# Optimization experiments

Hardware: AMD Instinct MI355X
Metric: run time of the kernel (lower is better)

The kernel has to match this reference:

```python
import jax, jax.numpy as jnp
import numpy as np

BIG = jnp.float32(9e15)


def _normalize(sim, mask):
    # min/max are taken over positions where mask == 0 (faithful to the torch code)
    mn = jnp.min(jnp.where(mask == 0.0, sim, BIG), axis=-1, keepdims=True)
    mx = jnp.max(jnp.where(mask == 0.0, sim, -BIG), axis=-1, keepdims=True)
    return (sim - mn) / (mx - mn)


def setup_inputs() -> dict:
    key = jax.random.key(0)
    k1, k2 = jax.random.split(key)
    B, M = 4096, 8192
    return {
        "similarity_matrix": jax.random.normal(k1, (B, B), dtype=jnp.float32),
        "memory_bank_matrix": jax.random.normal(k2, (B, M), dtype=jnp.float32),
        "num_neighbors": 32,
        "temperature": jnp.ones((), dtype=jnp.float32),
    }


def reference(similarity_matrix, memory_bank_matrix, num_neighbors, temperature):
    sim = similarity_matrix
    B = sim.shape[0]
    eye = jnp.eye(B, dtype=sim.dtype)

    # --- neighbor masks via top-k over off-diagonal similarities ---
    sim_noself = jnp.where(eye == 0.0, sim, -BIG)
    _, topk_idx = jax.lax.top_k(sim_noself, num_neighbors)       # [B, k]
    rows = jnp.broadcast_to(jnp.arange(B)[:, None], topk_idx.shape)
    neighbor_mask = jnp.zeros((B, B), dtype=sim.dtype).at[rows, topk_idx].set(1.0)
    extended_mask = eye.at[rows, topk_idx].set(1.0)

    # --- centrality from memory bank ---
    centrality = jnp.mean(memory_bank_matrix, axis=-1)           # [B]
    cent_exp = jnp.broadcast_to(centrality[None, :], (B, B))

    norm_sim = _normalize(sim, extended_mask)
    norm_cent = _normalize(cent_exp, extended_mask)

    adjusted = jnp.where(neighbor_mask == 1.0, norm_sim - norm_cent, -BIG)

    # --- positive weights ---
    pw = jax.nn.softmax(adjusted * temperature, axis=-1)
    pw = jnp.where(neighbor_mask == 1.0, pw, 0.0)
    pw = jnp.where(eye == 1.0, 1.0, pw)  # fill_diagonal_(1.0)

    # --- masked log-softmax loss ---
    masked_sim = jnp.where(extended_mask == 1.0, sim, -BIG)
    logp = jax.nn.log_softmax(masked_sim, axis=-1) * pw
    per_row = -jnp.sum(logp, axis=-1) / jnp.sum(pw, axis=-1)
    return jnp.mean(per_row)
```

## Files before the change

kernel.cpp:

```cpp
#include <hip/hip_runtime.h>
#include <cmath>


#define CAP 256
#define MAXIT 40

__device__ inline float wave_max_f(float x) {
#pragma unroll
    for (int off = 32; off > 0; off >>= 1) x = fmaxf(x, __shfl_xor(x, off, 64));
    return x;
}
__device__ inline float wave_min_f(float x) {
#pragma unroll
    for (int off = 32; off > 0; off >>= 1) x = fminf(x, __shfl_xor(x, off, 64));
    return x;
}
__device__ inline float wave_sum_f(float x) {
#pragma unroll
    for (int off = 32; off > 0; off >>= 1) x += __shfl_xor(x, off, 64);
    return x;
}
__device__ inline unsigned int wave_min_u32(unsigned int x) {
#pragma unroll
    for (int off = 32; off > 0; off >>= 1) {
        unsigned int o = (unsigned int)__shfl_xor((int)x, off, 64);
        x = (o < x) ? o : x;
    }
    return x;
}

__device__ inline unsigned int f_to_key(float f) {
    unsigned int u = __float_as_uint(f);
    return u ^ ((u & 0x80000000u) ? 0xFFFFFFFFu : 0x80000000u);
}
__device__ inline float key_to_f(unsigned int key) {
    unsigned int u = key ^ ((key & 0x80000000u) ? 0x80000000u : 0xFFFFFFFFu);
    return __uint_as_float(u);
}

__global__ __launch_bounds__(256)
void cent_kernel(const float* __restrict__ mem, float* __restrict__ cent, int M) {
    __shared__ float s[4];
    const int row = blockIdx.x;
    const float4* p = (const float4*)(mem + (size_t)row * M);
    const int n4 = M >> 2;
    float acc = 0.0f;
    int i = threadIdx.x;
    for (; i + 1792 < n4; i += 2048) {
        float4 q0 = p[i], q1 = p[i + 256], q2 = p[i + 512], q3 = p[i + 768];
        float4 q4 = p[i + 1024], q5 = p[i + 1280], q6 = p[i + 1536], q7 = p[i + 1792];
        acc += ((q0.x + q0.y) + (q0.z + q0.w)) + ((q1.x + q1.y) + (q1.z + q1.w))
             + ((q2.x + q2.y) + (q2.z + q2.w)) + ((q3.x + q3.y) + (q3.z + q3.w))
             + ((q4.x + q4.y) + (q4.z + q4.w)) + ((q5.x + q5.y) + (q5.z + q5.w))
             + ((q6.x + q6.y) + (q6.z + q6.w)) + ((q7.x + q7.y) + (q7.z + q7.w));
    }
    for (; i < n4; i += 256) {
        float4 q = p[i];
        acc += (q.x + q.y) + (q.z + q.w);
    }
    acc = wave_sum_f(acc);
    const int lane = threadIdx.x & 63, wid = threadIdx.x >> 6;
    if (lane == 0) s[wid] = acc;
    __syncthreads();
    if (threadIdx.x == 0) cent[row] = (s[0] + s[1] + s[2] + s[3]) / (float)M;
}

__global__ __launch_bounds__(256)
void row_loss_kernel(const float* __restrict__ sim,
                     const float* __restrict__ cent,
                     const int* __restrict__ knn,
                     const float* __restrict__ temp_p,
                     float* __restrict__ per_row, int B) {
    __shared__ __align__(16) unsigned long long cand[CAP];
    __shared__ unsigned long long s_sel[64];
    __shared__ unsigned long long s_p33;
    __shared__ unsigned int s_kmin[4];
    __shared__ float s_cmin[4], s_cmax[4];
    __shared__ float s_cmin2[4], s_cmax2[4];
    __shared__ unsigned int s_cnt;
    __shared__ float s_diag;

    const int row = blockIdx.x, tid = threadIdx.x;
    const int lane = tid & 63, wid = tid >> 6;
    const int   k    = knn[0];
    const float temp = temp_p[0];

    unsigned int keys[16];
    unsigned int kmin = 0xFFFFFFFFu;
    const float4* rp = (const float4*)(sim + (size_t)row * B);
#pragma unroll
    for (int c = 0; c < 4; ++c) {
        float4 q = rp[c * 256 + tid];
        float t[4] = {q.x, q.y, q.z, q.w};
#pragma unroll
        for (int m = 0; m < 4; ++m) {
            const int j = c * 1024 + tid * 4 + m;
            unsigned int key = f_to_key(t[m]);
            if (j == row) { s_diag = t[m]; key = 0u; }
            else if (key < kmin) kmin = key;
            keys[c * 4 + m] = key;
        }
    }
    { unsigned int w = wave_min_u32(kmin); if (lane == 0) s_kmin[wid] = w; }
    if (tid == 0) { s_cnt = 0; s_p33 = ((unsigned long long)1u) << 32; }

    unsigned int keyT = f_to_key(2.0f), loK = 0u, hiK = 0xFFFFFFFFu, cnt = 0;
    const unsigned int need = (unsigned int)k + 1u;
    float cmin, cmax;
    const float4* cp = (const float4*)cent;
    for (int it = 0; it < MAXIT; ++it) {
        cmin = INFINITY; cmax = -INFINITY;
        __syncthreads();
#pragma unroll
        for (int c = 0; c < 4; ++c) {
            float4 q = cp[c * 256 + tid];
            float t[4] = {q.x, q.y, q.z, q.w};
#pragma unroll
            for (int m = 0; m < 4; ++m) {
                const unsigned int key = keys[c * 4 + m];
                if (key == 0u) continue;
                if (key > keyT) {
                    const unsigned int pos = atomicAdd(&s_cnt, 1u);
                    if (pos < CAP)
                        cand[pos] = ((unsigned long long)key << 32) |
                                    (unsigned long long)(0xFFFFFFFFu -
                                        (unsigned int)(c * 1024 + tid * 4 + m));
                } else {
                    cmin = fminf(cmin, t[m]);
                    cmax = fmaxf(cmax, t[m]);
                }
            }
        }
        { float a = wave_min_f(cmin), b = wave_max_f(cmax);
          if (lane == 0) { s_cmin[wid] = a; s_cmax[wid] = b; } }
        __syncthreads();
        cnt = s_cnt;
        if (cnt >= need && cnt <= CAP) break;
        if (cnt < need) { hiK = keyT; keyT = loK + ((keyT - loK) >> 1); }
        else            { loK = keyT; keyT = keyT + ((hiK - keyT) >> 1); }
        if (tid == 0) s_cnt = 0;
    }

    {
        const unsigned int n = min(cnt, (unsigned int)CAP);
        const unsigned int uk = (unsigned int)k;
        unsigned long long own = 0ull;
        if ((unsigned int)tid < n) own = cand[tid];
        unsigned int r = 0;
        const ulonglong2* c2 = (const ulonglong2*)cand;
        const unsigned int np = n >> 1;
        for (unsigned int o = 0; o < np; ++o) {
            ulonglong2 pr = c2[o];
            r += (pr.x > own) ? 1u : 0u;
            r += (pr.y > own) ? 1u : 0u;
        }
        if (n & 1u) r += (cand[n - 1u] > own) ? 1u : 0u;

        float cmin2 = INFINITY, cmax2 = -INFINITY;
        if ((unsigned int)tid < n) {
            if (r < uk) s_sel[r] = own;
            else if (r == uk) s_p33 = own;
            if (r >= uk) {
                const int jj = (int)(0xFFFFFFFFu - (unsigned int)own);
                const float cv = cent[jj];
                cmin2 = fminf(cmin2, cv);
                cmax2 = fmaxf(cmax2, cv);
            }
        }
        cmin2 = wave_min_f(cmin2);
        cmax2 = wave_max_f(cmax2);
        if (lane == 0) { s_cmin2[wid] = cmin2; s_cmax2[wid] = cmax2; }
        __syncthreads();
    }
    if (wid != 0) return;

    {
        const float mn_c = fminf(
            fminf(fminf(s_cmin2[0], s_cmin2[1]), fminf(s_cmin2[2], s_cmin2[3])),
            fminf(fminf(s_cmin[0], s_cmin[1]), fminf(s_cmin[2], s_cmin[3])));
        const float mx_c = fmaxf(
            fmaxf(fmaxf(s_cmax2[0], s_cmax2[1]), fmaxf(s_cmax2[2], s_cmax2[3])),
            fmaxf(fmaxf(s_cmax[0], s_cmax[1]), fmaxf(s_cmax[2], s_cmax[3])));
        const unsigned int kminb =
            min(min(s_kmin[0], s_kmin[1]), min(s_kmin[2], s_kmin[3]));
        const float mn_s = key_to_f(kminb);
        const float mx_s = key_to_f((unsigned int)(s_p33 >> 32));

        const float sdiag = s_diag;
        const bool  act = (lane < k);
        const unsigned long long sel = act ? s_sel[lane] : 0ull;
        const float sj = act ? key_to_f((unsigned int)(sel >> 32)) : -INFINITY;
        const int   j  = act ? (int)(0xFFFFFFFFu - (unsigned int)sel) : 0;
        const float cj = cent[j];

        float a = -INFINITY;
        if (act) {
            const float ns = (sj - mn_s) / (mx_s - mn_s);
            const float nc = (cj - mn_c) / (mx_c - mn_c);
            a = (ns - nc) * temp;
        }
        const float am   = wave_max_f(a);
        const float e    = act ? expf(a - am) : 0.0f;
        const float esum = wave_sum_f(e);
        const float pw   = e / esum;

        const float m2  = fmaxf(wave_max_f(sj), sdiag);
        const float ex  = act ? expf(sj - m2) : 0.0f;
        const float lse = m2 + logf(wave_sum_f(ex) + expf(sdiag - m2));

        const float num = wave_sum_f(act ? pw * (sj - lse) : 0.0f) + (sdiag - lse);
        const float den = 1.0f + wave_sum_f(pw);
        if (lane == 0) per_row[row] = -num / den;
    }
}

__global__ __launch_bounds__(256)
void reduce_kernel(const float* __restrict__ per_row, float* __restrict__ out, int B) {
    __shared__ float s[4];
    float acc = 0.0f;
    const float4* p = (const float4*)per_row;
    const int n4 = B >> 2;
    for (int i = threadIdx.x; i < n4; i += 256) {
        float4 q = p[i];
        acc += (q.x + q.y) + (q.z + q.w);
    }
    acc = wave_sum_f(acc);
    const int lane = threadIdx.x & 63, wid = threadIdx.x >> 6;
    if (lane == 0) s[wid] = acc;
    __syncthreads();
    if (threadIdx.x == 0) out[0] = (s[0] + s[1] + s[2] + s[3]) / (float)B;
}

extern "C" void kernel_launch(void* const* d_in, const int* in_sizes, int n_in,
                              void* d_out, int out_size, void* d_ws, size_t ws_size,
                              hipStream_t stream) {
    const float* sim  = (const float*)d_in[0];
    const float* mem  = (const float*)d_in[1];
    const int*   knn  = (const int*)d_in[2];
    const float* temp = (const float*)d_in[3];
    float* out     = (float*)d_out;
    float* cent    = (float*)d_ws;
    float* per_row = (float*)d_ws + 4096;

    const int B = (int)(std::sqrt((double)in_sizes[0]) + 0.5);
    const int M = in_sizes[1] / B;

    cent_kernel<<<B, 256, 0, stream>>>(mem, cent, M);
    row_loss_kernel<<<B, 256, 0, stream>>>(sim, cent, knn, temp, per_row, B);
    reduce_kernel<<<1, 256, 0, stream>>>(per_row, out, B);
}
```

Measured before the change: 55.14 us.

## Process one row per wavefront with ballot-based candidate compaction

The row-loss kernel now assigns one row to each 64-lane wavefront instead of one per 256-thread block. This removes block-wide __syncthreads and LDS atomics, replacing the atomic compaction with ballot and mbcnt prefix compaction. The row is no longer cached in registers, so each threshold-search pass reloads the row and centrality from memory. The initial threshold is raised and the candidate cap is lowered to 128 per wave. Rows whose first guess misses the target range now pay extra full passes over global memory.

```diff
diff --git a/kernel.cpp b/kernel.cpp
--- a/kernel.cpp
+++ b/kernel.cpp
@@ -2,7 +2,7 @@
 #include <cmath>
 
 
-#define CAP 256
+#define CAPW 128
 #define MAXIT 40
 
 __device__ inline float wave_max_f(float x) {
@@ -28,6 +28,14 @@
     }
     return x;
 }
+__device__ inline unsigned int wave_max_u32(unsigned int x) {
+#pragma unroll
+    for (int off = 32; off > 0; off >>= 1) {
+        unsigned int o = (unsigned int)__shfl_xor((int)x, off, 64);
+        x = (o > x) ? o : x;
+    }
+    return x;
+}
 
 __device__ inline unsigned int f_to_key(float f) {
     unsigned int u = __float_as_uint(f);
@@ -36,6 +44,11 @@
 __device__ inline float key_to_f(unsigned int key) {
     unsigned int u = key ^ ((key & 0x80000000u) ? 0x80000000u : 0xFFFFFFFFu);
     return __uint_as_float(u);
+}
+
+__device__ inline unsigned int lane_prefix(unsigned long long mask) {
+    return __builtin_amdgcn_mbcnt_hi((unsigned int)(mask >> 32),
+           __builtin_amdgcn_mbcnt_lo((unsigned int)mask, 0u));
 }
 
 __global__ __launch_bounds__(256)
@@ -71,147 +84,173 @@
                      const int* __restrict__ knn,
                      const float* __restrict__ temp_p,
                      float* __restrict__ per_row, int B) {
-    __shared__ __align__(16) unsigned long long cand[CAP];
-    __shared__ unsigned long long s_sel[64];
-    __shared__ unsigned long long s_p33;
-    __shared__ unsigned int s_kmin[4];
-    __shared__ float s_cmin[4], s_cmax[4];
-    __shared__ float s_cmin2[4], s_cmax2[4];
-    __shared__ unsigned int s_cnt;
-    __shared__ float s_diag;
-
-    const int row = blockIdx.x, tid = threadIdx.x;
-    const int lane = tid & 63, wid = tid >> 6;
+    __shared__ __align__(16) unsigned long long cand[4][CAPW];
+    __shared__ __align__(16) unsigned long long ssel[4][64];
+
+    const int tid = threadIdx.x, lane = tid & 63, wid = tid >> 6;
+    const int row = (blockIdx.x << 2) + wid;
     const int   k    = knn[0];
     const float temp = temp_p[0];
-
-    unsigned int keys[16];
-    unsigned int kmin = 0xFFFFFFFFu;
+    const unsigned int uk = (unsigned int)k, need = uk + 1u;
+
     const float4* rp = (const float4*)(sim + (size_t)row * B);
-#pragma unroll
-    for (int c = 0; c < 4; ++c) {
-        float4 q = rp[c * 256 + tid];
-        float t[4] = {q.x, q.y, q.z, q.w};
-#pragma unroll
-        for (int m = 0; m < 4; ++m) {
-            const int j = c * 1024 + tid * 4 + m;
-            unsigned int key = f_to_key(t[m]);
-            if (j == row) { s_diag = t[m]; key = 0u; }
-            else if (key < kmin) kmin = key;
-            keys[c * 4 + m] = key;
-        }
-    }
-    { unsigned int w = wave_min_u32(kmin); if (lane == 0) s_kmin[wid] = w; }
-    if (tid == 0) { s_cnt = 0; s_p33 = ((unsigned long long)1u) << 32; }
-
-    unsigned int keyT = f_to_key(2.0f), loK = 0u, hiK = 0xFFFFFFFFu, cnt = 0;
-    const unsigned int need = (unsigned int)k + 1u;
-    float cmin, cmax;
     const float4* cp = (const float4*)cent;
-    for (int it = 0; it < MAXIT; ++it) {
+    unsigned long long* mycand = cand[wid];
+    unsigned long long* mysel  = ssel[wid];
+
+    float cmin, cmax, dval;
+    unsigned int kmin, wcnt;
+
+    auto pass = [&](unsigned int kT, bool wr) {
         cmin = INFINITY; cmax = -INFINITY;
-        __syncthreads();
-#pragma unroll
-        for (int c = 0; c < 4; ++c) {
-            float4 q = cp[c * 256 + tid];
-            float t[4] = {q.x, q.y, q.z, q.w};
-#pragma unroll
-            for (int m = 0; m < 4; ++m) {
-                const unsigned int key = keys[c * 4 + m];
-                if (key == 0u) continue;
-                if (key > keyT) {
-                    const unsigned int pos = atomicAdd(&s_cnt, 1u);
-                    if (pos < CAP)
-                        cand[pos] = ((unsigned long long)key << 32) |
-                                    (unsigned long long)(0xFFFFFFFFu -
-                                        (unsigned int)(c * 1024 + tid * 4 + m));
-                } else {
-                    cmin = fminf(cmin, t[m]);
-                    cmax = fmaxf(cmax, t[m]);
+        kmin = 0xFFFFFFFFu; dval = -INFINITY; wcnt = 0u;
+        for (int g = 0; g < 4; ++g) {
+            float4 sv[4], cw4[4];
+#pragma unroll
+            for (int u = 0; u < 4; ++u) sv[u] = rp[(g * 4 + u) * 64 + lane];
+#pragma unroll
+            for (int u = 0; u < 4; ++u) cw4[u] = cp[(g * 4 + u) * 64 + lane];
+#pragma unroll
+            for (int u = 0; u < 4; ++u) {
+                const int c = g * 4 + u;
+                const float tv[4] = {sv[u].x, sv[u].y, sv[u].z, sv[u].w};
+                const float cw[4] = {cw4[u].x, cw4[u].y, cw4[u].z, cw4[u].w};
+#pragma unroll
+                for (int m = 0; m < 4; ++m) {
+                    const int j = c * 256 + lane * 4 + m;
+                    unsigned int key = f_to_key(tv[m]);
+                    const bool isd = (j == row);
+                    if (isd) { dval = tv[m]; key = 0u; }
+                    else if (key < kmin) kmin = key;
+                    const bool p = (key > kT);
+                    const unsigned long long mask = __ballot(p);
+                    if (p) {
+                        if (wr) {
+                            const unsigned int pos = wcnt + lane_prefix(mask);
+                            if (pos < CAPW)
+                                mycand[pos] = ((unsigned long long)key << 32) |
+                                    (unsigned long long)(0xFFFFFFFFu - (unsigned int)j);
+                        }
+                    } else if (!isd) {
+                        cmin = fminf(cmin, cw[m]);
+                        cmax = fmaxf(cmax, cw[m]);
+                    }
+                    wcnt += (unsigned int)__popcll(mask);
                 }
             }
         }
-        { float a = wave_min_f(cmin), b = wave_max_f(cmax);
-          if (lane == 0) { s_cmin[wid] = a; s_cmax[wid] = b; } }
-        __syncthreads();
-        cnt = s_cnt;
-        if (cnt >= need && cnt <= CAP) break;
-        if (cnt < need) { hiK = keyT; keyT = loK + ((keyT - loK) >> 1); }
-        else            { loK = keyT; keyT = keyT + ((hiK - keyT) >> 1); }
-        if (tid == 0) s_cnt = 0;
-    }
-
-    {
-        const unsigned int n = min(cnt, (unsigned int)CAP);
-        const unsigned int uk = (unsigned int)k;
-        unsigned long long own = 0ull;
-        if ((unsigned int)tid < n) own = cand[tid];
-        unsigned int r = 0;
-        const ulonglong2* c2 = (const ulonglong2*)cand;
-        const unsigned int np = n >> 1;
-        for (unsigned int o = 0; o < np; ++o) {
-            ulonglong2 pr = c2[o];
-            r += (pr.x > own) ? 1u : 0u;
-            r += (pr.y > own) ? 1u : 0u;
-        }
-        if (n & 1u) r += (cand[n - 1u] > own) ? 1u : 0u;
-
-        float cmin2 = INFINITY, cmax2 = -INFINITY;
-        if ((unsigned int)tid < n) {
-            if (r < uk) s_sel[r] = own;
-            else if (r == uk) s_p33 = own;
-            if (r >= uk) {
-                const int jj = (int)(0xFFFFFFFFu - (unsigned int)own);
+    };
+
+    unsigned int keyT = f_to_key(2.2f);
+    pass(keyT, true);
+    unsigned int n = wcnt;
+    if (n < need || n > CAPW) {
+        unsigned int loK = 0u, hiK = 0xFFFFFFFFu;
+        for (int it = 0; it < MAXIT; ++it) {
+            if (n < need) { hiK = keyT; keyT = loK + ((keyT - loK) >> 1); }
+            else          { loK = keyT; keyT = keyT + ((hiK - keyT) >> 1); }
+            pass(keyT, false);
+            n = wcnt;
+            if (n >= need && n <= CAPW) break;
+        }
+        pass(keyT, true);
+        n = wcnt;
+        if (n > CAPW) n = CAPW;
+    }
+
+    const unsigned int kminb = wave_min_u32(kmin);
+    const float sdiag = wave_max_f(dval);
+    const float cminP = wave_min_f(cmin);
+    const float cmaxP = wave_max_f(cmax);
+
+    __builtin_amdgcn_wave_barrier();
+
+    unsigned long long own = mycand[lane];
+    unsigned long long own2 = 0ull;
+    unsigned int r = 0, r2 = 0;
+    const ulonglong2* c2 = (const ulonglong2*)mycand;
+    if (n <= 64u) {
+#pragma unroll
+        for (int o = 0; o < 32; ++o) {
+            const ulonglong2 pr = c2[o];
+            if ((unsigned int)(2 * o)     < n && pr.x > own) ++r;
+            if ((unsigned int)(2 * o + 1) < n && pr.y > own) ++r;
+        }
+    } else {
+        own2 = mycand[64 + lane];
+#pragma unroll
+        for (int o = 0; o < 64; ++o) {
+            const ulonglong2 pr = c2[o];
+            if ((unsigned int)(2 * o) < n) {
+                if (pr.x > own)  ++r;
+                if (pr.x > own2) ++r2;
+            }
+            if ((unsigned int)(2 * o + 1) < n) {
+                if (pr.y > own)  ++r;
+                if (pr.y > own2) ++r2;
+            }
+        }
+    }
+
+    float cmin2 = INFINITY, cmax2 = -INFINITY;
+    unsigned int p33k = 0u;
+    if ((unsigned int)lane < n) {
+        if (r < uk) mysel[r] = own;
+        else if (r == uk) p33k = (unsigned int)(own >> 32);
+        if (r >= uk) {
+            const int jj = (int)(0xFFFFFFFFu - (unsigned int)own);
+            const float cv = cent[jj];
+            cmin2 = fminf(cmin2, cv);
+            cmax2 = fmaxf(cmax2, cv);
+        }
+    }
+    if (n > 64u) {
+        const unsigned int t2 = (unsigned int)lane + 64u;
+        if (t2 < n) {
+            if (r2 < uk) mysel[r2] = own2;
+            else if (r2 == uk) p33k = (unsigned int)(own2 >> 32);
+            if (r2 >= uk) {
+                const int jj = (int)(0xFFFFFFFFu - (unsigned int)own2);
                 const float cv = cent[jj];
                 cmin2 = fminf(cmin2, cv);
                 cmax2 = fmaxf(cmax2, cv);
             }
         }
-        cmin2 = wave_min_f(cmin2);
-        cmax2 = wave_max_f(cmax2);
-        if (lane == 0) { s_cmin2[wid] = cmin2; s_cmax2[wid] = cmax2; }
-        __syncthreads();
-    }
-    if (wid != 0) return;
-
-    {
-        const float mn_c = fminf(
-            fminf(fminf(s_cmin2[0], s_cmin2[1]), fminf(s_cmin2[2], s_cmin2[3])),
-            fminf(fminf(s_cmin[0], s_cmin[1]), fminf(s_cmin[2], s_cmin[3])));
-        const float mx_c = fmaxf(
-            fmaxf(fmaxf(s_cmax2[0], s_cmax2[1]), fmaxf(s_cmax2[2], s_cmax2[3])),
-            fmaxf(fmaxf(s_cmax[0], s_cmax[1]), fmaxf(s_cmax[2], s_cmax[3])));
-        const unsigned int kminb =
-            min(min(s_kmin[0], s_kmin[1]), min(s_kmin[2], s_kmin[3]));
-        const float mn_s = key_to_f(kminb);
-        const float mx_s = key_to_f((unsigned int)(s_p33 >> 32));
-
-        const float sdiag = s_diag;
-        const bool  act = (lane < k);
-        const unsigned long long sel = act ? s_sel[lane] : 0ull;
-        const float sj = act ? key_to_f((unsigned int)(sel >> 32)) : -INFINITY;
-        const int   j  = act ? (int)(0xFFFFFFFFu - (unsigned int)sel) : 0;
-        const float cj = cent[j];
-
-        float a = -INFINITY;
-        if (act) {
-            const float ns = (sj - mn_s) / (mx_s - mn_s);
-            const float nc = (cj - mn_c) / (mx_c - mn_c);
-            a = (ns - nc) * temp;
-        }
-        const float am   = wave_max_f(a);
-        const float e    = act ? expf(a - am) : 0.0f;
-        const float esum = wave_sum_f(e);
-        const float pw   = e / esum;
-
-        const float m2  = fmaxf(wave_max_f(sj), sdiag);
-        const float ex  = act ? expf(sj - m2) : 0.0f;
-        const float lse = m2 + logf(wave_sum_f(ex) + expf(sdiag - m2));
-
-        const float num = wave_sum_f(act ? pw * (sj - lse) : 0.0f) + (sdiag - lse);
-        const float den = 1.0f + wave_sum_f(pw);
-        if (lane == 0) per_row[row] = -num / den;
-    }
+    }
+    p33k  = wave_max_u32(p33k);
+    cmin2 = wave_min_f(cmin2);
+    cmax2 = wave_max_f(cmax2);
+    __builtin_amdgcn_wave_barrier();
+
+    const float mn_c = fminf(cmin2, cminP);
+    const float mx_c = fmaxf(cmax2, cmaxP);
+    const float mn_s = key_to_f(kminb);
+    const float mx_s = key_to_f(p33k);
+
+    const bool act = (lane < k);
+    const unsigned long long sel = act ? mysel[lane] : 0ull;
+    const float sj = act ? key_to_f((unsigned int)(sel >> 32)) : -INFINITY;
+    const int   j  = act ? (int)(0xFFFFFFFFu - (unsigned int)sel) : 0;
+    const float cj = cent[j];
+
+    float a = -INFINITY;
+    if (act) {
+        const float ns = (sj - mn_s) / (mx_s - mn_s);
+        const float nc = (cj - mn_c) / (mx_c - mn_c);
+        a = (ns - nc) * temp;
+    }
+    const float am   = wave_max_f(a);
+    const float e    = act ? expf(a - am) : 0.0f;
+    const float esum = wave_sum_f(e);
+    const float pw   = e / esum;
+
+    const float m2  = fmaxf(key_to_f((unsigned int)(mysel[0] >> 32)), sdiag);
+    const float ex  = act ? expf(sj - m2) : 0.0f;
+    const float lse = m2 + logf(wave_sum_f(ex) + expf(sdiag - m2));
+
+    const float num = wave_sum_f(act ? pw * (sj - lse) : 0.0f) + (sdiag - lse);
+    const float den = 1.0f + wave_sum_f(pw);
+    if (lane == 0) per_row[row] = -num / den;
 }
 
 __global__ __launch_bounds__(256)
@@ -246,6 +285,6 @@
     const int M = in_sizes[1] / B;
 
     cent_kernel<<<B, 256, 0, stream>>>(mem, cent, M);
-    row_loss_kernel<<<B, 256, 0, stream>>>(sim, cent, knn, temp, per_row, B);
+    row_loss_kernel<<<B / 4, 256, 0, stream>>>(sim, cent, knn, temp, per_row, B);
     reduce_kernel<<<1, 256, 0, stream>>>(per_row, out, B);
 }
```

New measurement: 49.88 us (median of 2 runs). -9.5%, faster.
